# Kernel optimization log

Hardware: AMD Instinct MI355X
Metric: run time of the kernel (lower is better)

Reference implementation:

```python
import jax, jax.numpy as jnp
import numpy as np

B, IN, H, NC = 8192, 1024, 1024, 16
CS = H // NC  # chunk_size = 64


def cumsoftmax(x):
    # cumulative softmax along last dim
    return jnp.cumsum(jax.nn.softmax(x, axis=-1), axis=-1)


def setup_inputs() -> dict:
    key = jax.random.key(0)
    ks = jax.random.split(key, 9)
    s_ih = 1.0 / np.sqrt(IN)
    s_hh = 1.0 / np.sqrt(H)
    return {
        "x": jax.random.normal(ks[0], (B, IN), jnp.float32),
        "hx": jax.random.normal(ks[1], (B, H), jnp.float32),
        "cx": jax.random.normal(ks[2], (B, NC, CS), jnp.float32),
        "input_floor": jax.random.normal(ks[3], (B, NC), jnp.float32),
        "forget_floor": jax.random.normal(ks[4], (B, NC), jnp.float32),
        "W_ih": jax.random.uniform(ks[5], (4 * H, IN), jnp.float32, -s_ih, s_ih),
        "b_ih": jax.random.uniform(ks[6], (4 * H,), jnp.float32, -s_ih, s_ih),
        "W_hh": jax.random.uniform(ks[7], (4 * H, H), jnp.float32, -s_hh, s_hh),
        "b_hh": jax.random.uniform(ks[8], (4 * H,), jnp.float32, -s_hh, s_hh),
    }


def reference(x, hx, cx, input_floor, forget_floor, W_ih, b_ih, W_hh, b_hh):
    # dual GEMM (eval path: dropconnect=0.0 -> plain linear)
    gates = x @ W_ih.T + b_ih + hx @ W_hh.T + b_hh          # [B, 4H]
    g = gates.reshape(-1, NC * 4, CS)                        # [B, 4*NC, CS]
    outgate, cell, ingate, forgetgate = jnp.split(g, 4, axis=1)  # each [B, NC, CS]

    happy_in, sad_in = jnp.split(input_floor, 2, axis=1)     # [B, NC/2] each
    happy_fg, sad_fg = jnp.split(forget_floor, 2, axis=1)

    happy_cingate = cumsoftmax(happy_in)
    happy_cforgetgate = jnp.flip(cumsoftmax(jnp.flip(happy_fg, 1)), 1)
    sad_cingate = jnp.flip(cumsoftmax(jnp.flip(sad_in, 1)), 1)
    sad_cforgetgate = cumsoftmax(sad_fg)

    cingate = jnp.concatenate([happy_cingate, sad_cingate], axis=1)[:, :, None]      # [B, NC, 1]
    cforgetgate = jnp.concatenate([happy_cforgetgate, sad_cforgetgate], axis=1)[:, :, None]

    ingate = jax.nn.sigmoid(ingate)
    forgetgate = jax.nn.sigmoid(forgetgate)
    cell = jnp.tanh(cell)
    outgate = jax.nn.sigmoid(outgate)

    overlap = cforgetgate * cingate
    forgetgate = forgetgate * overlap + (cforgetgate - overlap)
    ingate = ingate * overlap + (cingate - overlap)

    cy = forgetgate * cx + ingate * cell                     # [B, NC, CS]
    hy = outgate * jnp.tanh(cy)
    return hy.reshape(-1, H), cy
```

## Files before the change

kernel.cpp:

```cpp
#include <hip/hip_runtime.h>
#include <hip/hip_bf16.h>


#define B_ROWS 8192
#define IN_DIM 1024
#define H_DIM  1024
#define NCHUNK 16
#define K_TOT  2048

#define BM   256
#define BN   256
#define BK   64
#define NKT  (K_TOT / BK)
#define THREADS 512

#define A_PACK_BYTES ((size_t)B_ROWS * K_TOT * 2)
#define W_PACK_BYTES ((size_t)16 * 256 * K_TOT * 2)

typedef __attribute__((ext_vector_type(4))) float  f32x4;
typedef __bf16 bf16x8 __attribute__((ext_vector_type(8)));

__device__ __forceinline__ float sigmoidf_(float x) {
    return 1.0f / (1.0f + __expf(-x));
}
__device__ __forceinline__ float tanhf_(float x) {
    float e = __expf(-2.0f * fabsf(x));
    float t = (1.0f - e) / (1.0f + e);
    return copysignf(t, x);
}

__device__ __forceinline__ void gload16(const __bf16* gsrc, __bf16* lds_dst) {
    __builtin_amdgcn_global_load_lds(
        (const __attribute__((address_space(1))) unsigned int*)gsrc,
        (__attribute__((address_space(3))) unsigned int*)lds_dst, 16, 0, 0);
}

__device__ __forceinline__ bf16x8 cvt8(f32x4 v0, f32x4 v1) {
    bf16x8 o;
    o[0] = (__bf16)v0.x; o[1] = (__bf16)v0.y; o[2] = (__bf16)v0.z; o[3] = (__bf16)v0.w;
    o[4] = (__bf16)v1.x; o[5] = (__bf16)v1.y; o[6] = (__bf16)v1.z; o[7] = (__bf16)v1.w;
    return o;
}

__global__ __launch_bounds__(256)
void pack_A(const float* __restrict__ x, const float* __restrict__ hx,
            __bf16* __restrict__ Abf)
{
    int idx = blockIdx.x * 256 + threadIdx.x;
    int row = idx >> 8;
    int c8  = (idx & 255) << 3;
    const float* src = (c8 < IN_DIM)
        ? (x  + (size_t)row * IN_DIM + c8)
        : (hx + (size_t)row * IN_DIM + (c8 - IN_DIM));
    f32x4 v0 = *reinterpret_cast<const f32x4*>(src);
    f32x4 v1 = *reinterpret_cast<const f32x4*>(src + 4);
    *reinterpret_cast<bf16x8*>(Abf + (size_t)row * K_TOT + c8) = cvt8(v0, v1);
}

__global__ __launch_bounds__(256)
void pack_W(const float* __restrict__ W_ih, const float* __restrict__ W_hh,
            __bf16* __restrict__ Wp)
{
    int idx = blockIdx.x * 256 + threadIdx.x;
    int k8  = (idx & 255) << 3;
    int n   = (idx >> 8) & 255;
    int bh  = idx >> 16;
    int g   = (n >> 4) & 3;
    int j   = (n >> 6) * 16 + (n & 15);
    int wr  = g * H_DIM + bh * 64 + j;
    const float* src = (k8 < IN_DIM)
        ? (W_ih + (size_t)wr * IN_DIM + k8)
        : (W_hh + (size_t)wr * IN_DIM + (k8 - IN_DIM));
    f32x4 v0 = *reinterpret_cast<const f32x4*>(src);
    f32x4 v1 = *reinterpret_cast<const f32x4*>(src + 4);
    *reinterpret_cast<bf16x8*>(Wp + ((size_t)bh * 256 + n) * K_TOT + k8) = cvt8(v0, v1);
}

__device__ __forceinline__ void stage_half(const __bf16* __restrict__ gbase, int kb,
                                           __bf16* lbase, int row0, int tid) {
    #pragma unroll
    for (int i = 0; i < 2; ++i) {
        int e   = i * 4096 + tid * 8;
        int row = row0 + (e >> 6);
        int kd  = e & 63;
        gload16(gbase + (size_t)row * K_TOT + kb + (kd ^ ((row & 7) << 3)), lbase + e);
    }
}

#define SWZ(r, k) ((r) * 64 + ((k) ^ (((r) & 7) << 3)))

#define LDB(Bs) { \
    _Pragma("unroll") \
    for (int fn = 0; fn < 4; ++fn) { \
        int br = wcol + fn * 16 + lr; \
        bfr[fn][0] = *reinterpret_cast<const bf16x8*>(&(Bs)[SWZ(br, lh * 8)]); \
        bfr[fn][1] = *reinterpret_cast<const bf16x8*>(&(Bs)[SWZ(br, 32 + lh * 8)]); \
    } }

#define LDA(As, q) { \
    int ar = wrow + (q) * 32 + lr; \
    af[0][0] = *reinterpret_cast<const bf16x8*>(&(As)[SWZ(ar, lh * 8)]); \
    af[0][1] = *reinterpret_cast<const bf16x8*>(&(As)[SWZ(ar, 32 + lh * 8)]); \
    af[1][0] = *reinterpret_cast<const bf16x8*>(&(As)[SWZ(ar + 16, lh * 8)]); \
    af[1][1] = *reinterpret_cast<const bf16x8*>(&(As)[SWZ(ar + 16, 32 + lh * 8)]); \
    }

#define PH_PRE \
    asm volatile("" ::: "memory"); \
    __builtin_amdgcn_s_barrier(); \
    asm volatile("s_waitcnt lgkmcnt(0)" ::: "memory"); \
    __builtin_amdgcn_sched_barrier(0);

#define MF(q) { \
    __builtin_amdgcn_s_setprio(1); \
    _Pragma("unroll") \
    for (int fn = 0; fn < 4; ++fn) { \
        acc[2*(q)][fn]   = __builtin_amdgcn_mfma_f32_16x16x32_bf16(af[0][0], bfr[fn][0], acc[2*(q)][fn],   0,0,0); \
        acc[2*(q)][fn]   = __builtin_amdgcn_mfma_f32_16x16x32_bf16(af[0][1], bfr[fn][1], acc[2*(q)][fn],   0,0,0); \
        acc[2*(q)+1][fn] = __builtin_amdgcn_mfma_f32_16x16x32_bf16(af[1][0], bfr[fn][0], acc[2*(q)+1][fn], 0,0,0); \
        acc[2*(q)+1][fn] = __builtin_amdgcn_mfma_f32_16x16x32_bf16(af[1][1], bfr[fn][1], acc[2*(q)+1][fn], 0,0,0); \
    } \
    __builtin_amdgcn_s_setprio(0); \
    __builtin_amdgcn_sched_barrier(0); \
}

#define PH_POST \
    asm volatile("" ::: "memory"); \
    __builtin_amdgcn_s_barrier();

#define PH_POSTV \
    asm volatile("s_waitcnt vmcnt(4)" ::: "memory"); \
    __builtin_amdgcn_s_barrier();

__global__ __launch_bounds__(THREADS, 2)
void onlstm_gemm8(const __bf16* __restrict__ Abf, const __bf16* __restrict__ Wp,
                  const float* __restrict__ cx,
                  const float* __restrict__ input_floor,
                  const float* __restrict__ forget_floor,
                  const float* __restrict__ b_ih, const float* __restrict__ b_hh,
                  float* __restrict__ out)
{
    __shared__ __align__(16) __bf16 lds[65536];
    __shared__ float ci_s[BM], cf_s[BM], bias_s[BN];

    const int tid = threadIdx.x;
    const int n0  = blockIdx.x;
    const int bm  = (n0 & 7) * 4 + ((n0 >> 3) & 3);
    const int bh  = n0 >> 5;
    const int h0  = bh * 64;
    const int nc  = bh;

    if (tid < BM) {
        {
            int g = (tid >> 4) & 3;
            int j = (tid >> 6) * 16 + (tid & 15);
            int wrr = g * H_DIM + h0 + j;
            bias_s[tid] = b_ih[wrr] + b_hh[wrr];
        }
        int b = bm * BM + tid;
        const int off = (nc < 8) ? 0 : 8;
        const int ic  = (nc < 8) ? nc : (nc - 8);
        const float* pin = input_floor  + (size_t)b * NCHUNK + off;
        const float* pfg = forget_floor + (size_t)b * NCHUNK + off;
        float vi[8], vf[8];
        float mi = -1e30f, mf = -1e30f;
        #pragma unroll
        for (int t = 0; t < 8; ++t) {
            vi[t] = pin[t]; vf[t] = pfg[t];
            mi = fmaxf(mi, vi[t]); mf = fmaxf(mf, vf[t]);
        }
        float si = 0.f, sf = 0.f;
        #pragma unroll
        for (int t = 0; t < 8; ++t) {
            vi[t] = __expf(vi[t] - mi); vf[t] = __expf(vf[t] - mf);
            si += vi[t]; sf += vf[t];
        }
        float pi = 0.f, pf = 0.f;
        #pragma unroll
        for (int t = 0; t < 8; ++t) { if (t <= ic) { pi += vi[t]; pf += vf[t]; } }
        float suf_i = si - pi + vi[ic];
        float suf_f = sf - pf + vf[ic];
        float civ, cfv;
        if (nc < 8) { civ = pi / si;    cfv = suf_f / sf; }
        else        { civ = suf_i / si; cfv = pf / sf;    }
        ci_s[tid] = civ; cf_s[tid] = cfv;
    }

    const __bf16* Arow = Abf + (size_t)(bm * BM) * K_TOT;
    const __bf16* Wblk = Wp  + (size_t)bh * 256 * K_TOT;
    __bf16* const A0p = lds;
    __bf16* const B0p = lds + 16384;
    __bf16* const A1p = lds + 32768;
    __bf16* const B1p = lds + 49152;

    stage_half(Arow, 0,  A0p,        0,   tid);
    stage_half(Arow, 0,  A0p + 8192, 128, tid);
    stage_half(Wblk, 0,  B0p,        0,   tid);
    stage_half(Wblk, 0,  B0p + 8192, 128, tid);
    stage_half(Wblk, BK, B1p,        0,   tid);
    stage_half(Wblk, BK, B1p + 8192, 128, tid);
    asm volatile("s_waitcnt lgkmcnt(0)" ::: "memory");
    asm volatile("s_waitcnt vmcnt(0)"   ::: "memory");
    __builtin_amdgcn_s_barrier();
    asm volatile("" ::: "memory");

    f32x4  acc[8][4];
    #pragma unroll
    for (int i = 0; i < 8; ++i)
        #pragma unroll
        for (int j = 0; j < 4; ++j) acc[i][j] = (f32x4){0.f, 0.f, 0.f, 0.f};
    bf16x8 af[2][2];
    bf16x8 bfr[4][2];

    const int l    = tid & 63;
    const int wid  = tid >> 6;
    const int wrw  = wid >> 2;
    const int wc   = wid & 3;
    const int lr   = l & 15;
    const int lh   = l >> 4;
    const int wrow = wrw * 128;
    const int wcol = wc * 64;

    #pragma unroll 1
    for (int it = 0; it < NKT / 2; ++it) {
        const int t = 2 * it;
        LDB(B0p); LDA(A0p, 0);
        stage_half(Arow, ((t + 1) & 31) * BK, A1p,        0,   tid);
        PH_PRE; MF(0); PH_POST;
        LDA(A0p, 1);
        stage_half(Arow, ((t + 1) & 31) * BK, A1p + 8192, 128, tid);
        PH_PRE; MF(1); PH_POST;
        LDA(A0p, 2);
        stage_half(Wblk, ((t + 2) & 31) * BK, B0p,        0,   tid);
        PH_PRE; MF(2); PH_POST;
        LDA(A0p, 3);
        stage_half(Wblk, ((t + 2) & 31) * BK, B0p + 8192, 128, tid);
        PH_PRE; MF(3); PH_POSTV;
        LDB(B1p); LDA(A1p, 0);
        stage_half(Arow, ((t + 2) & 31) * BK, A0p,        0,   tid);
        PH_PRE; MF(0); PH_POST;
        LDA(A1p, 1);
        stage_half(Arow, ((t + 2) & 31) * BK, A0p + 8192, 128, tid);
        PH_PRE; MF(1); PH_POST;
        LDA(A1p, 2);
        stage_half(Wblk, ((t + 3) & 31) * BK, B1p,        0,   tid);
        PH_PRE; MF(2); PH_POST;
        LDA(A1p, 3);
        stage_half(Wblk, ((t + 3) & 31) * BK, B1p + 8192, 128, tid);
        PH_PRE; MF(3); PH_POSTV;
    }
    asm volatile("s_waitcnt vmcnt(0)" ::: "memory");

    const size_t CY_OFF = (size_t)B_ROWS * H_DIM;
    const int hcol = h0 + wc * 16 + lr;
    #pragma unroll
    for (int m = 0; m < 8; ++m) {
        #pragma unroll
        for (int r = 0; r < 4; ++r) {
            int rt = wrow + m * 16 + lh * 4 + r;
            int b  = bm * BM + rt;
            float civ = ci_s[rt], cfv = cf_s[rt];
            float ovl = cfv * civ;
            float og = acc[m][0][r] + bias_s[wcol + lr];
            float cg = acc[m][1][r] + bias_s[wcol + 16 + lr];
            float ig = acc[m][2][r] + bias_s[wcol + 32 + lr];
            float fg = acc[m][3][r] + bias_s[wcol + 48 + lr];
            float i_s = sigmoidf_(ig);
            float f_s = sigmoidf_(fg);
            float c_t = tanhf_(cg);
            float o_s = sigmoidf_(og);
            float fq = f_s * ovl + (cfv - ovl);
            float iq = i_s * ovl + (civ - ovl);
            float cxv = cx[(size_t)b * H_DIM + hcol];
            float cyv = fq * cxv + iq * c_t;
            float hyv = o_s * tanhf_(cyv);
            out[(size_t)b * H_DIM + hcol] = hyv;
            out[CY_OFF + (size_t)b * H_DIM + hcol] = cyv;
        }
    }
}

extern "C" void kernel_launch(void* const* d_in, const int* in_sizes, int n_in,
                              void* d_out, int out_size, void* d_ws, size_t ws_size,
                              hipStream_t stream) {
    const float* x            = (const float*)d_in[0];
    const float* hx           = (const float*)d_in[1];
    const float* cx           = (const float*)d_in[2];
    const float* input_floor  = (const float*)d_in[3];
    const float* forget_floor = (const float*)d_in[4];
    const float* W_ih         = (const float*)d_in[5];
    const float* b_ih         = (const float*)d_in[6];
    const float* W_hh         = (const float*)d_in[7];
    const float* b_hh         = (const float*)d_in[8];
    float* out = (float*)d_out;

    __bf16* Abf = (__bf16*)d_ws;
    __bf16* Wp  = (__bf16*)((char*)d_ws + A_PACK_BYTES);
    pack_A<<<B_ROWS, 256, 0, stream>>>(x, hx, Abf);
    pack_W<<<16 * 256, 256, 0, stream>>>(W_ih, W_hh, Wp);
    onlstm_gemm8<<<512, THREADS, 0, stream>>>(
        Abf, Wp, cx, input_floor, forget_floor, b_ih, b_hh, out);
}
```

Baseline: 160.4 us.

## Merge pack kernels and halve barriers per MFMA phase in GEMM loop

Combines the two bf16 pack kernels into a single launch, saving one kernel launch and its tail. In the main GEMM loop, each phase now uses one barrier instead of two. Staging loads are regrouped so the A tile is issued in the first phase and the B tile in the next two. The MFMA order is changed to run across k-steps, and the prologue waits only on part of the outstanding loads. This trims synchronisation overhead, but relies on the vmcnt accounting staying correct, with risk of races if load counts are off.

```diff
diff --git a/kernel.cpp b/kernel.cpp
--- a/kernel.cpp
+++ b/kernel.cpp
@@ -43,37 +43,33 @@
 }
 
 __global__ __launch_bounds__(256)
-void pack_A(const float* __restrict__ x, const float* __restrict__ hx,
-            __bf16* __restrict__ Abf)
+void pack_AW(const float* __restrict__ x, const float* __restrict__ hx,
+             const float* __restrict__ W_ih, const float* __restrict__ W_hh,
+             __bf16* __restrict__ Abf, __bf16* __restrict__ Wp)
 {
-    int idx = blockIdx.x * 256 + threadIdx.x;
-    int row = idx >> 8;
-    int c8  = (idx & 255) << 3;
-    const float* src = (c8 < IN_DIM)
-        ? (x  + (size_t)row * IN_DIM + c8)
-        : (hx + (size_t)row * IN_DIM + (c8 - IN_DIM));
-    f32x4 v0 = *reinterpret_cast<const f32x4*>(src);
-    f32x4 v1 = *reinterpret_cast<const f32x4*>(src + 4);
-    *reinterpret_cast<bf16x8*>(Abf + (size_t)row * K_TOT + c8) = cvt8(v0, v1);
-}
-
-__global__ __launch_bounds__(256)
-void pack_W(const float* __restrict__ W_ih, const float* __restrict__ W_hh,
-            __bf16* __restrict__ Wp)
-{
-    int idx = blockIdx.x * 256 + threadIdx.x;
-    int k8  = (idx & 255) << 3;
-    int n   = (idx >> 8) & 255;
-    int bh  = idx >> 16;
-    int g   = (n >> 4) & 3;
-    int j   = (n >> 6) * 16 + (n & 15);
-    int wr  = g * H_DIM + bh * 64 + j;
-    const float* src = (k8 < IN_DIM)
-        ? (W_ih + (size_t)wr * IN_DIM + k8)
-        : (W_hh + (size_t)wr * IN_DIM + (k8 - IN_DIM));
-    f32x4 v0 = *reinterpret_cast<const f32x4*>(src);
-    f32x4 v1 = *reinterpret_cast<const f32x4*>(src + 4);
-    *reinterpret_cast<bf16x8*>(Wp + ((size_t)bh * 256 + n) * K_TOT + k8) = cvt8(v0, v1);
+    const int bid = blockIdx.x;
+    const int c8  = threadIdx.x << 3;
+    if (bid < B_ROWS) {
+        const float* src = (c8 < IN_DIM)
+            ? (x  + (size_t)bid * IN_DIM + c8)
+            : (hx + (size_t)bid * IN_DIM + (c8 - IN_DIM));
+        f32x4 v0 = *reinterpret_cast<const f32x4*>(src);
+        f32x4 v1 = *reinterpret_cast<const f32x4*>(src + 4);
+        *reinterpret_cast<bf16x8*>(Abf + (size_t)bid * K_TOT + c8) = cvt8(v0, v1);
+    } else {
+        const int r  = bid - B_ROWS;
+        const int bh = r >> 8;
+        const int n  = r & 255;
+        const int g  = (n >> 4) & 3;
+        const int j  = (n >> 6) * 16 + (n & 15);
+        const int wr = g * H_DIM + bh * 64 + j;
+        const float* src = (c8 < IN_DIM)
+            ? (W_ih + (size_t)wr * IN_DIM + c8)
+            : (W_hh + (size_t)wr * IN_DIM + (c8 - IN_DIM));
+        f32x4 v0 = *reinterpret_cast<const f32x4*>(src);
+        f32x4 v1 = *reinterpret_cast<const f32x4*>(src + 4);
+        *reinterpret_cast<bf16x8*>(Wp + (size_t)r * K_TOT + c8) = cvt8(v0, v1);
+    }
 }
 
 __device__ __forceinline__ void stage_half(const __bf16* __restrict__ gbase, int kb,
@@ -105,32 +101,32 @@
     af[1][1] = *reinterpret_cast<const bf16x8*>(&(As)[SWZ(ar + 16, 32 + lh * 8)]); \
     }
 
-#define PH_PRE \
-    asm volatile("" ::: "memory"); \
+#define WBAR \
+    asm volatile("s_waitcnt lgkmcnt(0)" ::: "memory"); \
+    __builtin_amdgcn_sched_barrier(0); \
     __builtin_amdgcn_s_barrier(); \
+    __builtin_amdgcn_sched_barrier(0);
+
+#define WBARV \
     asm volatile("s_waitcnt lgkmcnt(0)" ::: "memory"); \
+    asm volatile("s_waitcnt vmcnt(4)"   ::: "memory"); \
+    __builtin_amdgcn_sched_barrier(0); \
+    __builtin_amdgcn_s_barrier(); \
     __builtin_amdgcn_sched_barrier(0);
 
 #define MF(q) { \
     __builtin_amdgcn_s_setprio(1); \
     _Pragma("unroll") \
-    for (int fn = 0; fn < 4; ++fn) { \
-        acc[2*(q)][fn]   = __builtin_amdgcn_mfma_f32_16x16x32_bf16(af[0][0], bfr[fn][0], acc[2*(q)][fn],   0,0,0); \
-        acc[2*(q)][fn]   = __builtin_amdgcn_mfma_f32_16x16x32_bf16(af[0][1], bfr[fn][1], acc[2*(q)][fn],   0,0,0); \
-        acc[2*(q)+1][fn] = __builtin_amdgcn_mfma_f32_16x16x32_bf16(af[1][0], bfr[fn][0], acc[2*(q)+1][fn], 0,0,0); \
-        acc[2*(q)+1][fn] = __builtin_amdgcn_mfma_f32_16x16x32_bf16(af[1][1], bfr[fn][1], acc[2*(q)+1][fn], 0,0,0); \
+    for (int ks = 0; ks < 2; ++ks) { \
+        _Pragma("unroll") \
+        for (int fn = 0; fn < 4; ++fn) { \
+            acc[2*(q)][fn]   = __builtin_amdgcn_mfma_f32_16x16x32_bf16(af[0][ks], bfr[fn][ks], acc[2*(q)][fn],   0,0,0); \
+            acc[2*(q)+1][fn] = __builtin_amdgcn_mfma_f32_16x16x32_bf16(af[1][ks], bfr[fn][ks], acc[2*(q)+1][fn], 0,0,0); \
+        } \
     } \
     __builtin_amdgcn_s_setprio(0); \
     __builtin_amdgcn_sched_barrier(0); \
 }
-
-#define PH_POST \
-    asm volatile("" ::: "memory"); \
-    __builtin_amdgcn_s_barrier();
-
-#define PH_POSTV \
-    asm volatile("s_waitcnt vmcnt(4)" ::: "memory"); \
-    __builtin_amdgcn_s_barrier();
 
 __global__ __launch_bounds__(THREADS, 2)
 void onlstm_gemm8(const __bf16* __restrict__ Abf, const __bf16* __restrict__ Wp,
@@ -200,7 +196,7 @@
     stage_half(Wblk, BK, B1p,        0,   tid);
     stage_half(Wblk, BK, B1p + 8192, 128, tid);
     asm volatile("s_waitcnt lgkmcnt(0)" ::: "memory");
-    asm volatile("s_waitcnt vmcnt(0)"   ::: "memory");
+    asm volatile("s_waitcnt vmcnt(4)"   ::: "memory");
     __builtin_amdgcn_s_barrier();
     asm volatile("" ::: "memory");
 
@@ -226,30 +222,31 @@
         const int t = 2 * it;
         LDB(B0p); LDA(A0p, 0);
         stage_half(Arow, ((t + 1) & 31) * BK, A1p,        0,   tid);
-        PH_PRE; MF(0); PH_POST;
+        stage_half(Arow, ((t + 1) & 31) * BK, A1p + 8192, 128, tid);
+        WBAR; MF(0);
         LDA(A0p, 1);
-        stage_half(Arow, ((t + 1) & 31) * BK, A1p + 8192, 128, tid);
-        PH_PRE; MF(1); PH_POST;
+        stage_half(Wblk, ((t + 2) & 31) * BK, B0p,        0,   tid);
+        WBAR; MF(1);
         LDA(A0p, 2);
-        stage_half(Wblk, ((t + 2) & 31) * BK, B0p,        0,   tid);
-        PH_PRE; MF(2); PH_POST;
+        stage_half(Wblk, ((t + 2) & 31) * BK, B0p + 8192, 128, tid);
+        WBAR; MF(2);
         LDA(A0p, 3);
-        stage_half(Wblk, ((t + 2) & 31) * BK, B0p + 8192, 128, tid);
-        PH_PRE; MF(3); PH_POSTV;
+        WBARV; MF(3);
         LDB(B1p); LDA(A1p, 0);
         stage_half(Arow, ((t + 2) & 31) * BK, A0p,        0,   tid);
-        PH_PRE; MF(0); PH_POST;
+        stage_half(Arow, ((t + 2) & 31) * BK, A0p + 8192, 128, tid);
+        WBAR; MF(0);
         LDA(A1p, 1);
-        stage_half(Arow, ((t + 2) & 31) * BK, A0p + 8192, 128, tid);
-        PH_PRE; MF(1); PH_POST;
+        stage_half(Wblk, ((t + 3) & 31) * BK, B1p,        0,   tid);
+        WBAR; MF(1);
         LDA(A1p, 2);
-        stage_half(Wblk, ((t + 3) & 31) * BK, B1p,        0,   tid);
-        PH_PRE; MF(2); PH_POST;
+        stage_half(Wblk, ((t + 3) & 31) * BK, B1p + 8192, 128, tid);
+        WBAR; MF(2);
         LDA(A1p, 3);
-        stage_half(Wblk, ((t + 3) & 31) * BK, B1p + 8192, 128, tid);
-        PH_PRE; MF(3); PH_POSTV;
+        WBARV; MF(3);
     }
     asm volatile("s_waitcnt vmcnt(0)" ::: "memory");
+    __builtin_amdgcn_s_barrier();
 
     const size_t CY_OFF = (size_t)B_ROWS * H_DIM;
     const int hcol = h0 + wc * 16 + lr;
@@ -296,8 +293,7 @@
 
     __bf16* Abf = (__bf16*)d_ws;
     __bf16* Wp  = (__bf16*)((char*)d_ws + A_PACK_BYTES);
-    pack_A<<<B_ROWS, 256, 0, stream>>>(x, hx, Abf);
-    pack_W<<<16 * 256, 256, 0, stream>>>(W_ih, W_hh, Wp);
+    pack_AW<<<B_ROWS + 16 * 256, 256, 0, stream>>>(x, hx, W_ih, W_hh, Abf, Wp);
     onlstm_gemm8<<<512, THREADS, 0, stream>>>(
         Abf, Wp, cx, input_floor, forget_floor, b_ih, b_hh, out);
 }
```

After: 157.5 us. No clear change (-1.8%).
